# Kernel optimization log

Hardware: AMD Instinct MI355X
Metric: run time of the kernel (lower is better)

Reference implementation:

```python
import jax, jax.numpy as jnp
import numpy as np

B, S, D = 2, 2048, 1024
H, L = 16, 512
DH = D // H
LN_EPS = 1e-5


def setup_inputs() -> dict:
    key = jax.random.key(0)
    ks = jax.random.split(key, 6)
    w = 0.02  # init scale for weights
    return {
        "x": jax.random.normal(ks[0], (B, S, D), jnp.float32),
        "W_q": jax.random.normal(ks[1], (D, D), jnp.float32) * w,
        "W_dkv": jax.random.normal(ks[2], (L, D), jnp.float32) * w,
        "W_uk": jax.random.normal(ks[3], (D, L), jnp.float32) * w,
        "W_uv": jax.random.normal(ks[4], (D, L), jnp.float32) * w,
        "W_o": jax.random.normal(ks[5], (D, D), jnp.float32) * w,
        "ln_gamma": jnp.ones((L,), jnp.float32),
        "ln_beta": jnp.zeros((L,), jnp.float32),
    }


def reference(x, W_q, W_dkv, W_uk, W_uv, W_o, ln_gamma, ln_beta):
    # latent KV: LayerNorm(x @ W_dkv^T)  -> [B, S, L]
    c = x @ W_dkv.T
    mu = jnp.mean(c, axis=-1, keepdims=True)
    var = jnp.mean((c - mu) ** 2, axis=-1, keepdims=True)
    c_kv = (c - mu) * jax.lax.rsqrt(var + LN_EPS) * ln_gamma + ln_beta

    # absorbed key projection: (W_q @ W_uk) viewed per head  -> [H, DH, L]
    absorbed_k = (W_q @ W_uk).reshape(H, DH, L)

    # q is raw x reshaped per head (W_q absorbed)  -> [B, S, H, DH]
    q = x.reshape(B, S, H, DH)
    tmp = jnp.einsum('bshd,hdl->bhsl', q, absorbed_k)         # [B,H,S,L]
    scores = jnp.einsum('bhsl,btl->bhst', tmp, c_kv) / np.sqrt(DH)

    # causal mask (past_length = 0, no kv_cache -> S_full == S)
    mask = jnp.tril(jnp.ones((S, S), bool))
    scores = jnp.where(mask[None, None], scores, -1e30)
    attn = jax.nn.softmax(scores, axis=-1)                    # [B,H,S,S]

    # values decompressed from latent  -> [B, S, H, DH]
    v = (c_kv @ W_uv.T).reshape(B, S, H, DH)
    ctx = jnp.einsum('bhst,bthd->bshd', attn, v).reshape(B, S, D)
    out = ctx @ W_o.T
    return out, c_kv
```

## Files before the change

kernel.cpp:

```cpp
#include <hip/hip_runtime.h>


typedef __attribute__((ext_vector_type(4))) float f32x4;
typedef __attribute__((ext_vector_type(8))) unsigned short u16x8;
typedef __attribute__((ext_vector_type(4))) unsigned short u16x4;
typedef __attribute__((ext_vector_type(8))) __bf16 bf16x8;

__device__ __forceinline__ unsigned short f2bf(float f) {
  unsigned int u = __builtin_bit_cast(unsigned int, f);
  u += 0x7FFFu + ((u >> 16) & 1u);
  return (unsigned short)(u >> 16);
}
__device__ __forceinline__ unsigned short f2bf_rz(float f) {
  return (unsigned short)(__builtin_bit_cast(unsigned int, f) >> 16);
}
__device__ __forceinline__ float bf2f(unsigned short u) {
  return __builtin_bit_cast(float, (unsigned int)u << 16);
}

__device__ __forceinline__ f32x4 mfma16(u16x8 a, u16x8 b, f32x4 c) {
  return __builtin_amdgcn_mfma_f32_16x16x32_bf16(
      __builtin_bit_cast(bf16x8, a), __builtin_bit_cast(bf16x8, b), c, 0, 0, 0);
}

__device__ __forceinline__ void gload_lds16(const void* g, void* l) {
  __builtin_amdgcn_global_load_lds(
      (const __attribute__((address_space(1))) unsigned int*)g,
      (__attribute__((address_space(3))) unsigned int*)l, 16, 0, 0);
}

__global__ __launch_bounds__(256)
void fused_cvt(const float* __restrict__ x, unsigned short* __restrict__ xb,
               const float* __restrict__ wq, unsigned short* __restrict__ wqb,
               const float* __restrict__ wdkv, unsigned short* __restrict__ wdkvb,
               const float* __restrict__ wuv, unsigned short* __restrict__ wuvb,
               const float* __restrict__ wo, unsigned short* __restrict__ wob) {
  const int total = 1048576 + 262144 + 131072 + 131072 + 262144;
  for (int i = blockIdx.x * 256 + threadIdx.x; i < total; i += gridDim.x * 256) {
    const float* src; unsigned short* dst; int off;
    if (i < 1048576)      { src = x;    dst = xb;    off = i; }
    else if (i < 1310720) { src = wq;   dst = wqb;   off = i - 1048576; }
    else if (i < 1441792) { src = wdkv; dst = wdkvb; off = i - 1310720; }
    else if (i < 1572864) { src = wuv;  dst = wuvb;  off = i - 1441792; }
    else                  { src = wo;   dst = wob;   off = i - 1572864; }
    float4 v = ((const float4*)src)[off];
    u16x4 o;
    o[0] = f2bf(v.x); o[1] = f2bf(v.y); o[2] = f2bf(v.z); o[3] = f2bf(v.w);
    ((u16x4*)dst)[off] = o;
  }
}

__global__ __launch_bounds__(256) void transpose_cvt(const float* __restrict__ in,
                                                     unsigned short* __restrict__ out) {
  __shared__ float t[64][65];
  int r0 = blockIdx.y * 64, c0 = blockIdx.x * 64;
  int lr = threadIdx.x >> 4, lc = (threadIdx.x & 15) * 4;
#pragma unroll
  for (int i = 0; i < 4; i++) {
    int row = lr + i * 16;
    float4 v = *(const float4*)(in + (size_t)(r0 + row) * 512 + c0 + lc);
    t[row][lc] = v.x; t[row][lc + 1] = v.y; t[row][lc + 2] = v.z; t[row][lc + 3] = v.w;
  }
  __syncthreads();
#pragma unroll
  for (int i = 0; i < 4; i++) {
    int oc = lr + i * 16;
    u16x4 o;
    o[0] = f2bf(t[lc + 0][oc]); o[1] = f2bf(t[lc + 1][oc]);
    o[2] = f2bf(t[lc + 2][oc]); o[3] = f2bf(t[lc + 3][oc]);
    *(u16x4*)(out + (size_t)(c0 + oc) * 1024 + r0 + lc) = o;
  }
}

template <int MODE, int IM, int JF, int MINW>
__global__ __launch_bounds__(256, MINW)
void gemm_bt(const unsigned short* __restrict__ A, const unsigned short* __restrict__ B,
             void* __restrict__ C1, void* __restrict__ C2,
             int M, int N, int K, int lda, int ldb, int ldc) {
  constexpr int BM = IM * 32, BN = JF * 32;
  __shared__ __align__(16) unsigned short sA[2][BM * 64];
  __shared__ __align__(16) unsigned short sB[2][BN * 64];
  const int tid = threadIdx.x;
  const int w = tid >> 6, ln = tid & 63;
  const int m0 = blockIdx.y * BM, n0 = blockIdx.x * BN;
  const int wm = (w >> 1) * (IM * 16), wn = (w & 1) * (JF * 16);
  const int c16 = ln & 15, g = ln >> 4;
  f32x4 zero = {0.f, 0.f, 0.f, 0.f};
  f32x4 acc[IM][JF];
#pragma unroll
  for (int i = 0; i < IM; i++)
#pragma unroll
    for (int j = 0; j < JF; j++) acc[i][j] = zero;

#define STAGE_G(kt, bf)                                                        \
  {                                                                            \
    _Pragma("unroll") for (int l = 0; l < BM / 32; l++) {                      \
      int c = l * 256 + tid;                                                   \
      int row = c >> 3, pc = c & 7;                                            \
      gload_lds16(A + (size_t)(m0 + row) * lda + (kt) + ((pc ^ (row & 7)) << 3),\
                  (char*)&sA[bf][0] + (l * 256 + w * 64) * 16);                \
    }                                                                          \
    _Pragma("unroll") for (int l = 0; l < BN / 32; l++) {                      \
      int c = l * 256 + tid;                                                   \
      int row = c >> 3, pc = c & 7;                                            \
      gload_lds16(B + (size_t)(n0 + row) * ldb + (kt) + ((pc ^ (row & 7)) << 3),\
                  (char*)&sB[bf][0] + (l * 256 + w * 64) * 16);                \
    }                                                                          \
  }

  STAGE_G(0, 0);
  __syncthreads();
  int bf = 0;
  for (int kt = 0; kt < K; kt += 64) {
    if (kt + 64 < K) STAGE_G(kt + 64, bf ^ 1);
    u16x8 af[IM][2], bfr[JF][2];
#pragma unroll
    for (int i = 0; i < IM; i++) {
      int ra = wm + i * 16 + c16;
#pragma unroll
      for (int kk = 0; kk < 2; kk++)
        af[i][kk] = *(const u16x8*)((const char*)&sA[bf][0] + ra * 128 +
                                    ((((kk << 2) + g) ^ (ra & 7)) << 4));
    }
#pragma unroll
    for (int j = 0; j < JF; j++) {
      int rb = wn + j * 16 + c16;
#pragma unroll
      for (int kk = 0; kk < 2; kk++)
        bfr[j][kk] = *(const u16x8*)((const char*)&sB[bf][0] + rb * 128 +
                                     ((((kk << 2) + g) ^ (rb & 7)) << 4));
    }
#pragma unroll
    for (int kk = 0; kk < 2; kk++)
#pragma unroll
      for (int i = 0; i < IM; i++)
#pragma unroll
        for (int j = 0; j < JF; j++)
          acc[i][j] = mfma16(af[i][kk], bfr[j][kk], acc[i][j]);
    __syncthreads();
    bf ^= 1;
  }
#undef STAGE_G
  const int row0 = m0 + wm + g * 4;
  const int col0 = n0 + wn + c16;
  if (MODE == 1) {
    float* C = (float*)C1;
#pragma unroll
    for (int i = 0; i < IM; i++)
#pragma unroll
      for (int j = 0; j < JF; j++)
#pragma unroll
        for (int r = 0; r < 4; r++)
          C[(size_t)(row0 + i * 16 + r) * ldc + col0 + j * 16] = acc[i][j][r];
  } else if (MODE == 0) {
    unsigned short* C = (unsigned short*)C1;
#pragma unroll
    for (int i = 0; i < IM; i++)
#pragma unroll
      for (int j = 0; j < JF; j++)
#pragma unroll
        for (int r = 0; r < 4; r++)
          C[(size_t)(row0 + i * 16 + r) * ldc + col0 + j * 16] = f2bf(acc[i][j][r]);
  } else {
    if (n0 < 1024) {
      unsigned short* C = (unsigned short*)C1;
#pragma unroll
      for (int i = 0; i < IM; i++)
#pragma unroll
        for (int j = 0; j < JF; j++)
#pragma unroll
          for (int r = 0; r < 4; r++)
            C[(size_t)(row0 + i * 16 + r) * ldc + col0 + j * 16] = f2bf(acc[i][j][r]);
    } else {
      unsigned short* C = (unsigned short*)C2;
#pragma unroll
      for (int i = 0; i < IM; i++)
#pragma unroll
        for (int j = 0; j < JF; j++) {
          u16x4 t4;
#pragma unroll
          for (int r = 0; r < 4; r++) t4[r] = f2bf(acc[i][j][r]);
          *(u16x4*)(C + (size_t)(col0 + j * 16 - 1024) * 4096 + row0 + i * 16) = t4;
        }
    }
  }
}

__global__ __launch_bounds__(256)
void ln_rows(const float* __restrict__ cin, const float* __restrict__ gamma,
             const float* __restrict__ beta, float* __restrict__ of32,
             unsigned short* __restrict__ obf) {
  int row = blockIdx.x * 4 + (threadIdx.x >> 6);
  int ln = threadIdx.x & 63;
  const float* r = cin + (size_t)row * 512 + ln * 8;
  float4 a = *(const float4*)r;
  float4 b = *(const float4*)(r + 4);
  float xv[8] = {a.x, a.y, a.z, a.w, b.x, b.y, b.z, b.w};
  float s = 0.f, q = 0.f;
#pragma unroll
  for (int j = 0; j < 8; j++) { s += xv[j]; q += xv[j] * xv[j]; }
#pragma unroll
  for (int m = 1; m < 64; m <<= 1) { s += __shfl_xor(s, m); q += __shfl_xor(q, m); }
  float mu = s * (1.f / 512.f);
  float var = q * (1.f / 512.f) - mu * mu;
  float rs = rsqrtf(var + 1e-5f);
  float gm[8], bt[8];
  *(float4*)&gm[0] = *(const float4*)(gamma + ln * 8);
  *(float4*)&gm[4] = *(const float4*)(gamma + ln * 8 + 4);
  *(float4*)&bt[0] = *(const float4*)(beta + ln * 8);
  *(float4*)&bt[4] = *(const float4*)(beta + ln * 8 + 4);
  float o[8];
#pragma unroll
  for (int j = 0; j < 8; j++) o[j] = (xv[j] - mu) * rs * gm[j] + bt[j];
  float4 o0 = {o[0], o[1], o[2], o[3]}, o1 = {o[4], o[5], o[6], o[7]};
  *(float4*)(of32 + (size_t)row * 512 + ln * 8) = o0;
  *(float4*)(of32 + (size_t)row * 512 + ln * 8 + 4) = o1;
  u16x8 ob;
#pragma unroll
  for (int j = 0; j < 8; j++) ob[j] = f2bf(o[j]);
  *(u16x8*)(obf + (size_t)row * 512 + ln * 8) = ob;
}

__global__ __launch_bounds__(256, 3)
void mla_attn5(const unsigned short* __restrict__ kabs,
               const unsigned short* __restrict__ xq,
               const unsigned short* __restrict__ vT,
               unsigned short* __restrict__ Opart,
               float* __restrict__ Lpart) {
  __shared__ __align__(16) unsigned short sK[2][64 * 64];
  __shared__ __align__(16) unsigned short sVT[2][64 * 64];
  __shared__ __align__(16) unsigned short sP[4][16 * 72];
  const int tid = threadIdx.x, w = tid >> 6, ln = tid & 63;
  const int g = ln >> 4, c16 = ln & 15;
  const int bh = blockIdx.y;
  const int b = bh >> 4, h = bh & 15;
  int cid = blockIdx.x, qb, ch;
  if (cid < 8)       { qb = cid;                 ch = 0; }
  else if (cid < 24) { qb = 8 + ((cid - 8) >> 1);  ch = (cid - 8) & 1; }
  else if (cid < 48) { qb = 16 + (cid - 24) / 3;   ch = (cid - 24) % 3; }
  else               { qb = 24 + ((cid - 48) >> 2); ch = (cid - 48) & 3; }
  const int ts = ch * 8;
  const int te = min(ts + 8, qb + 1);
  const int q0 = qb * 64;
  const int qw = q0 + w * 16;
  const size_t rowb = (size_t)b * 2048;

  u16x8 qf[2];
  {
    const unsigned short* qp = xq + (rowb + qw + c16) * 1024 + h * 64 + g * 8;
    qf[0] = *(const u16x8*)(qp);
    qf[1] = *(const u16x8*)(qp + 32);
  }
  f32x4 zero = {0.f, 0.f, 0.f, 0.f};
  f32x4 o[4] = {zero, zero, zero, zero};
  float lsum[4] = {0.f, 0.f, 0.f, 0.f};
  const float SC = 0.18033688011112042f;
  const float M0 = 8.f;
  unsigned short* Pw = &sP[w][0];
  const unsigned short* kb_g = kabs + rowb * 1024 + h * 64;
  const unsigned short* vb_g = vT + (size_t)(h * 64) * 4096 + rowb;

#define STAGE_A(tt, bfi)                                                       \
  {                                                                            \
    int t0s = (tt) * 64;                                                       \
    _Pragma("unroll") for (int l = 0; l < 2; l++) {                            \
      int c = l * 256 + tid;                                                   \
      int row = c >> 3, pc = c & 7;                                            \
      gload_lds16(kb_g + (size_t)(t0s + row) * 1024 + ((pc ^ (row & 7)) << 3), \
                  (char*)&sK[bfi][0] + (l * 256 + w * 64) * 16);               \
    }                                                                          \
    _Pragma("unroll") for (int l = 0; l < 2; l++) {                            \
      int c = l * 256 + tid;                                                   \
      int row = c >> 3, pc = c & 7;                                            \
      gload_lds16(vb_g + (size_t)row * 4096 + t0s + ((pc ^ (row & 7)) << 3),   \
                  (char*)&sVT[bfi][0] + (l * 256 + w * 64) * 16);              \
    }                                                                          \
  }

  STAGE_A(ts, 0);
  __syncthreads();
  int bf = 0;
  for (int tt = ts; tt < te; tt++) {
    const int t0 = tt * 64;
    if (tt + 1 < te) STAGE_A(tt + 1, bf ^ 1);
    f32x4 s[4];
#pragma unroll
    for (int nt = 0; nt < 4; nt++) {
      int t = nt * 16 + c16;
      int sw = t & 7;
      const char* kb = (const char*)&sK[bf][0] + t * 128;
      f32x4 a = zero;
      a = mfma16(qf[0], *(const u16x8*)(kb + ((g ^ sw) << 4)), a);
      a = mfma16(qf[1], *(const u16x8*)(kb + (((4 + g) ^ sw) << 4)), a);
      s[nt] = a;
    }
    if (t0 + 63 <= qw) {
#pragma unroll
      for (int nt = 0; nt < 4; nt++)
#pragma unroll
        for (int r = 0; r < 4; r++) {
          float p = exp2f(s[nt][r] * SC - M0);
          lsum[r] += p;
          s[nt][r] = p;
        }
    } else {
#pragma unroll
      for (int nt = 0; nt < 4; nt++) {
        int tcol = t0 + nt * 16 + c16;
#pragma unroll
        for (int r = 0; r < 4; r++) {
          float p = (tcol <= qw + g * 4 + r) ? exp2f(s[nt][r] * SC - M0) : 0.f;
          lsum[r] += p;
          s[nt][r] = p;
        }
      }
    }
#pragma unroll
    for (int nt = 0; nt < 4; nt++)
#pragma unroll
      for (int r = 0; r < 4; r++)
        Pw[(g * 4 + r) * 72 + nt * 16 + c16] = f2bf_rz(s[nt][r]);
#pragma unroll
    for (int ks = 0; ks < 2; ks++) {
      u16x8 pa = *(const u16x8*)((const char*)Pw + c16 * 144 + ks * 64 + g * 16);
#pragma unroll
      for (int dt = 0; dt < 4; dt++) {
        int d = dt * 16 + c16;
        const char* vb = (const char*)&sVT[bf][0] + d * 128 +
                         ((((ks << 2) + g) ^ (d & 7)) << 4);
        o[dt] = mfma16(pa, *(const u16x8*)vb, o[dt]);
      }
    }
    __syncthreads();
    bf ^= 1;
  }
#undef STAGE_A
  unsigned short* op = Opart + ((size_t)bh * 80 + cid) * 4096;
  float* lp = Lpart + ((size_t)bh * 80 + cid) * 64;
#pragma unroll
  for (int r = 0; r < 4; r++) {
    float t = lsum[r];
    t += __shfl_xor(t, 1); t += __shfl_xor(t, 2);
    t += __shfl_xor(t, 4); t += __shfl_xor(t, 8);
    int ql = w * 16 + g * 4 + r;
    if (c16 == 0) lp[ql] = t;
#pragma unroll
    for (int dt = 0; dt < 4; dt++)
      op[ql * 64 + dt * 16 + c16] = f2bf(o[dt][r]);
  }
}

__global__ __launch_bounds__(256)
void attn_combine(const unsigned short* __restrict__ Opart,
                  const float* __restrict__ Lpart,
                  unsigned short* __restrict__ ctx) {
  const int qb = blockIdx.x, bh = blockIdx.y;
  const int b = bh >> 4, h = bh & 15;
  const int ncq = (qb >> 3) + 1;
  const int g8 = qb >> 3;
  const int start = (g8 == 0 ? 0 : (g8 == 1 ? 8 : (g8 == 2 ? 24 : 48)));
  const int cid0 = start + (qb & 7) * ncq;
  const int q = threadIdx.x >> 2;
  const int d0 = (threadIdx.x & 3) * 16;
  float acc[16];
#pragma unroll
  for (int j = 0; j < 16; j++) acc[j] = 0.f;
  float lacc = 0.f;
  for (int c = 0; c < ncq; c++) {
    size_t base = (size_t)bh * 80 + cid0 + c;
    lacc += Lpart[base * 64 + q];
    const unsigned short* op = Opart + base * 4096 + q * 64 + d0;
    u16x8 v0 = *(const u16x8*)(op);
    u16x8 v1 = *(const u16x8*)(op + 8);
#pragma unroll
    for (int j = 0; j < 8; j++) { acc[j] += bf2f(v0[j]); acc[8 + j] += bf2f(v1[j]); }
  }
  float inv = 1.f / lacc;
  u16x8 o0, o1;
#pragma unroll
  for (int j = 0; j < 8; j++) { o0[j] = f2bf(acc[j] * inv); o1[j] = f2bf(acc[8 + j] * inv); }
  unsigned short* cp = ctx + ((size_t)b * 2048 + qb * 64 + q) * 1024 + h * 64 + d0;
  *(u16x8*)(cp) = o0;
  *(u16x8*)(cp + 8) = o1;
}

extern "C" void kernel_launch(void* const* d_in, const int* in_sizes, int n_in,
                              void* d_out, int out_size, void* d_ws, size_t ws_size,
                              hipStream_t stream) {
  const float* x    = (const float*)d_in[0];
  const float* Wq   = (const float*)d_in[1];
  const float* Wdkv = (const float*)d_in[2];
  const float* Wuk  = (const float*)d_in[3];
  const float* Wuv  = (const float*)d_in[4];
  const float* Wo   = (const float*)d_in[5];
  const float* gam  = (const float*)d_in[6];
  const float* bet  = (const float*)d_in[7];
  float* out_f = (float*)d_out;
  float* ckv_f = out_f + (size_t)4096 * 1024;

  char* ws = (char*)d_ws;
  unsigned short* xb     = (unsigned short*)(ws);
  unsigned short* wq_b   = (unsigned short*)(ws + 8388608);
  unsigned short* wdkv_b = (unsigned short*)(ws + 10485760);
  unsigned short* wukT_b = (unsigned short*)(ws + 11534336);
  unsigned short* akt_b  = (unsigned short*)(ws + 12582912);
  unsigned short* wuv_b  = (unsigned short*)(ws + 13631488);
  unsigned short* wo_b   = (unsigned short*)(ws + 14680064);
  unsigned short* ckv_b  = (unsigned short*)(ws + 16777216);
  float*          c_f    = (float*)(ws + 20971520);
  unsigned short* kabs   = (unsigned short*)(ws + 29360128);
  unsigned short* vT     = (unsigned short*)(ws + 37748736);
  unsigned short* ctx_b  = (unsigned short*)(ws + 46137344);
  unsigned short* Opart  = (unsigned short*)(ws + 54525952);
  float*          Lpart  = (float*)(ws + 75497472);

  fused_cvt<<<2048, 256, 0, stream>>>(x, xb, Wq, wq_b, Wdkv, wdkv_b,
                                      Wuv, wuv_b, Wo, wo_b);
  transpose_cvt<<<dim3(8, 16), 256, 0, stream>>>(Wuk, wukT_b);

  gemm_bt<1, 2, 2, 4><<<dim3(8, 64), 256, 0, stream>>>(xb, wdkv_b, c_f, nullptr,
                                                       4096, 512, 1024, 1024, 1024, 512);
  ln_rows<<<1024, 256, 0, stream>>>(c_f, gam, bet, ckv_f, ckv_b);
  gemm_bt<0, 1, 2, 4><<<dim3(8, 32), 256, 0, stream>>>(wq_b, wukT_b, akt_b, nullptr,
                                                       1024, 512, 1024, 1024, 1024, 512);
  gemm_bt<3, 4, 4, 2><<<dim3(16, 32), 256, 0, stream>>>(ckv_b, akt_b, kabs, vT,
                                                        4096, 2048, 512, 512, 512, 1024);
  mla_attn5<<<dim3(80, 32), 256, 0, stream>>>(kabs, xb, vT, Opart, Lpart);
  attn_combine<<<dim3(32, 32), 256, 0, stream>>>(Opart, Lpart, ctx_b);
  gemm_bt<1, 2, 4, 3><<<dim3(8, 64), 256, 0, stream>>>(ctx_b, wo_b, out_f, nullptr,
                                                       4096, 1024, 1024, 1024, 1024, 1024);
}
```

Before: 205.0 us.

## Fold W_uk transpose into conversion kernel and shrink attention P staging buffer

The separate transpose_cvt launch is merged into fused_cvt as 128 extra blocks, removing one kernel launch. The attention kernel now stages the probability tile to LDS in two 32-column halves using a smaller per-wave buffer. The launch bound is raised from 3 to 4 waves per SIMD to increase occupancy. The trade-off is tighter register pressure and an extra write/read round of P through LDS per tile. fused_cvt also now declares a 64x65 float shared array for every block, including the conversion-only ones.

```diff
diff --git a/kernel.cpp b/kernel.cpp
--- a/kernel.cpp
+++ b/kernel.cpp
@@ -34,9 +34,33 @@
                const float* __restrict__ wq, unsigned short* __restrict__ wqb,
                const float* __restrict__ wdkv, unsigned short* __restrict__ wdkvb,
                const float* __restrict__ wuv, unsigned short* __restrict__ wuvb,
-               const float* __restrict__ wo, unsigned short* __restrict__ wob) {
+               const float* __restrict__ wo, unsigned short* __restrict__ wob,
+               const float* __restrict__ wuk, unsigned short* __restrict__ wukT) {
+  __shared__ float t[64][65];
+  if (blockIdx.x >= 2048) {
+    int bid = blockIdx.x - 2048;
+    int c0 = (bid & 7) * 64;
+    int r0 = (bid >> 3) * 64;
+    int lr = threadIdx.x >> 4, lc = (threadIdx.x & 15) * 4;
+#pragma unroll
+    for (int i = 0; i < 4; i++) {
+      int row = lr + i * 16;
+      float4 v = *(const float4*)(wuk + (size_t)(r0 + row) * 512 + c0 + lc);
+      t[row][lc] = v.x; t[row][lc + 1] = v.y; t[row][lc + 2] = v.z; t[row][lc + 3] = v.w;
+    }
+    __syncthreads();
+#pragma unroll
+    for (int i = 0; i < 4; i++) {
+      int oc = lr + i * 16;
+      u16x4 o;
+      o[0] = f2bf(t[lc + 0][oc]); o[1] = f2bf(t[lc + 1][oc]);
+      o[2] = f2bf(t[lc + 2][oc]); o[3] = f2bf(t[lc + 3][oc]);
+      *(u16x4*)(wukT + (size_t)(c0 + oc) * 1024 + r0 + lc) = o;
+    }
+    return;
+  }
   const int total = 1048576 + 262144 + 131072 + 131072 + 262144;
-  for (int i = blockIdx.x * 256 + threadIdx.x; i < total; i += gridDim.x * 256) {
+  for (int i = blockIdx.x * 256 + threadIdx.x; i < total; i += 2048 * 256) {
     const float* src; unsigned short* dst; int off;
     if (i < 1048576)      { src = x;    dst = xb;    off = i; }
     else if (i < 1310720) { src = wq;   dst = wqb;   off = i - 1048576; }
@@ -47,28 +71,6 @@
     u16x4 o;
     o[0] = f2bf(v.x); o[1] = f2bf(v.y); o[2] = f2bf(v.z); o[3] = f2bf(v.w);
     ((u16x4*)dst)[off] = o;
-  }
-}
-
-__global__ __launch_bounds__(256) void transpose_cvt(const float* __restrict__ in,
-                                                     unsigned short* __restrict__ out) {
-  __shared__ float t[64][65];
-  int r0 = blockIdx.y * 64, c0 = blockIdx.x * 64;
-  int lr = threadIdx.x >> 4, lc = (threadIdx.x & 15) * 4;
-#pragma unroll
-  for (int i = 0; i < 4; i++) {
-    int row = lr + i * 16;
-    float4 v = *(const float4*)(in + (size_t)(r0 + row) * 512 + c0 + lc);
-    t[row][lc] = v.x; t[row][lc + 1] = v.y; t[row][lc + 2] = v.z; t[row][lc + 3] = v.w;
-  }
-  __syncthreads();
-#pragma unroll
-  for (int i = 0; i < 4; i++) {
-    int oc = lr + i * 16;
-    u16x4 o;
-    o[0] = f2bf(t[lc + 0][oc]); o[1] = f2bf(t[lc + 1][oc]);
-    o[2] = f2bf(t[lc + 2][oc]); o[3] = f2bf(t[lc + 3][oc]);
-    *(u16x4*)(out + (size_t)(c0 + oc) * 1024 + r0 + lc) = o;
   }
 }
 
@@ -221,15 +223,15 @@
   *(u16x8*)(obf + (size_t)row * 512 + ln * 8) = ob;
 }
 
-__global__ __launch_bounds__(256, 3)
-void mla_attn5(const unsigned short* __restrict__ kabs,
+__global__ __launch_bounds__(256, 4)
+void mla_attn6(const unsigned short* __restrict__ kabs,
                const unsigned short* __restrict__ xq,
                const unsigned short* __restrict__ vT,
                unsigned short* __restrict__ Opart,
                float* __restrict__ Lpart) {
   __shared__ __align__(16) unsigned short sK[2][64 * 64];
   __shared__ __align__(16) unsigned short sVT[2][64 * 64];
-  __shared__ __align__(16) unsigned short sP[4][16 * 72];
+  __shared__ __align__(16) unsigned short sP[4][16 * 40];
   const int tid = threadIdx.x, w = tid >> 6, ln = tid & 63;
   const int g = ln >> 4, c16 = ln & 15;
   const int bh = blockIdx.y;
@@ -316,18 +318,18 @@
       }
     }
 #pragma unroll
-    for (int nt = 0; nt < 4; nt++)
-#pragma unroll
-      for (int r = 0; r < 4; r++)
-        Pw[(g * 4 + r) * 72 + nt * 16 + c16] = f2bf_rz(s[nt][r]);
-#pragma unroll
-    for (int ks = 0; ks < 2; ks++) {
-      u16x8 pa = *(const u16x8*)((const char*)Pw + c16 * 144 + ks * 64 + g * 16);
+    for (int half = 0; half < 2; half++) {
+#pragma unroll
+      for (int ntl = 0; ntl < 2; ntl++)
+#pragma unroll
+        for (int r = 0; r < 4; r++)
+          Pw[(g * 4 + r) * 40 + ntl * 16 + c16] = f2bf_rz(s[half * 2 + ntl][r]);
+      u16x8 pa = *(const u16x8*)((const char*)Pw + c16 * 80 + g * 16);
 #pragma unroll
       for (int dt = 0; dt < 4; dt++) {
         int d = dt * 16 + c16;
         const char* vb = (const char*)&sVT[bf][0] + d * 128 +
-                         ((((ks << 2) + g) ^ (d & 7)) << 4);
+                         ((((half << 2) + g) ^ (d & 7)) << 4);
         o[dt] = mfma16(pa, *(const u16x8*)vb, o[dt]);
       }
     }
@@ -414,9 +416,8 @@
   unsigned short* Opart  = (unsigned short*)(ws + 54525952);
   float*          Lpart  = (float*)(ws + 75497472);
 
-  fused_cvt<<<2048, 256, 0, stream>>>(x, xb, Wq, wq_b, Wdkv, wdkv_b,
-                                      Wuv, wuv_b, Wo, wo_b);
-  transpose_cvt<<<dim3(8, 16), 256, 0, stream>>>(Wuk, wukT_b);
+  fused_cvt<<<2176, 256, 0, stream>>>(x, xb, Wq, wq_b, Wdkv, wdkv_b,
+                                      Wuv, wuv_b, Wo, wo_b, Wuk, wukT_b);
 
   gemm_bt<1, 2, 2, 4><<<dim3(8, 64), 256, 0, stream>>>(xb, wdkv_b, c_f, nullptr,
                                                        4096, 512, 1024, 1024, 1024, 512);
@@ -425,7 +426,7 @@
                                                        1024, 512, 1024, 1024, 1024, 512);
   gemm_bt<3, 4, 4, 2><<<dim3(16, 32), 256, 0, stream>>>(ckv_b, akt_b, kabs, vT,
                                                         4096, 2048, 512, 512, 512, 1024);
-  mla_attn5<<<dim3(80, 32), 256, 0, stream>>>(kabs, xb, vT, Opart, Lpart);
+  mla_attn6<<<dim3(80, 32), 256, 0, stream>>>(kabs, xb, vT, Opart, Lpart);
   attn_combine<<<dim3(32, 32), 256, 0, stream>>>(Opart, Lpart, ctx_b);
   gemm_bt<1, 2, 4, 3><<<dim3(8, 64), 256, 0, stream>>>(ctx_b, wo_b, out_f, nullptr,
                                                        4096, 1024, 1024, 1024, 1024, 1024);
```

Result: faster. 199.0 us (-2.9%).
